# Kernel optimization log

Hardware: AMD Instinct MI355X
Metric: run time of the kernel (lower is better)

## Reference

```python
import jax, jax.numpy as jnp
import numpy as np
from jax import lax

WINDOW_SIZE = 11
SIGMA = 1.5
DATA_RANGE = 2.0


def _gauss_1d(size, sigma):
    coords = np.arange(size, dtype=np.float32) - size // 2
    g = np.exp(-coords ** 2 / (2.0 * sigma ** 2))
    g /= g.sum()
    return jnp.asarray(g)


def _gaussian_filter_2d(x, window):
    # x: (N, C, H, W); separable depthwise Gaussian blur
    C = x.shape[1]
    pad = window.shape[0] // 2
    win_h = jnp.tile(window.reshape(1, 1, 1, -1), (C, 1, 1, 1))  # (C,1,1,K)
    win_v = jnp.tile(window.reshape(1, 1, -1, 1), (C, 1, 1, 1))  # (C,1,K,1)
    dn = ('NCHW', 'OIHW', 'NCHW')
    out = lax.conv_general_dilated(x, win_h, window_strides=(1, 1),
                                   padding=((0, 0), (pad, pad)),
                                   dimension_numbers=dn, feature_group_count=C)
    out = lax.conv_general_dilated(out, win_v, window_strides=(1, 1),
                                   padding=((pad, pad), (0, 0)),
                                   dimension_numbers=dn, feature_group_count=C)
    return out


def _ssim_2d(x, y):
    C1 = (0.01 * DATA_RANGE) ** 2
    C2 = (0.03 * DATA_RANGE) ** 2
    window = _gauss_1d(WINDOW_SIZE, SIGMA).astype(x.dtype)
    mu_x = _gaussian_filter_2d(x, window)
    mu_y = _gaussian_filter_2d(y, window)
    mu_x_sq = mu_x * mu_x
    mu_y_sq = mu_y * mu_y
    mu_xy = mu_x * mu_y
    sigma_x_sq = jnp.maximum(_gaussian_filter_2d(x * x, window) - mu_x_sq, 0.0)
    sigma_y_sq = jnp.maximum(_gaussian_filter_2d(y * y, window) - mu_y_sq, 0.0)
    sigma_xy = _gaussian_filter_2d(x * y, window) - mu_xy
    ssim_map = ((2.0 * mu_xy + C1) * (2.0 * sigma_xy + C2)) / (
        (mu_x_sq + mu_y_sq + C1) * (sigma_x_sq + sigma_y_sq + C2))
    return ssim_map.mean()


def setup_inputs() -> dict:
    key = jax.random.key(0)
    k1, k2 = jax.random.split(key)
    pred = jax.random.normal(k1, (16, 3, 512, 512), dtype=jnp.float32)
    target = jax.random.normal(k2, (16, 3, 512, 512), dtype=jnp.float32)
    return {"pred": pred, "target": target}


def reference(pred, target):
    return 1.0 - _ssim_2d(pred, target)
```

## Files before the change

kernel.cpp:

```cpp
#include <hip/hip_runtime.h>
#include <math.h>


typedef _Float16 f16x8 __attribute__((ext_vector_type(8)));
typedef _Float16 f16x4 __attribute__((ext_vector_type(4)));
typedef float f32x4 __attribute__((ext_vector_type(4)));
typedef _Float16 h2 __attribute__((ext_vector_type(2)));

#define RAWP 88
#define NPIX (16 * 3 * 512 * 512)
#define NBLOCKS (48 * 16 * 8)

union U4 { f16x4 v; h2 p[2]; };
union U8 { f16x8 v; h2 p[4]; };
union UB { unsigned u[4]; f16x8 v; };
union UP { h2 h; unsigned u; };

static __device__ __forceinline__ h2 pkrtz(float a, float b) {
    auto r = __builtin_amdgcn_cvt_pkrtz(a, b);
    union { decltype(r) f; h2 h; } x; x.f = r; return x.h;
}
static __device__ __forceinline__ unsigned pk_u32(float a, float b) {
    UP x; x.h = pkrtz(a, b); return x.u;
}

struct alignas(16) BandTabs { float bh[64][8]; float wv[64][8]; };
static constexpr BandTabs mk_tabs() {
    constexpr float GW[11] = {
        0.00102838f, 0.00759876f, 0.03600026f, 0.10936083f, 0.21300567f,
        0.26601190f, 0.21300567f, 0.10936083f, 0.03600026f, 0.00759876f,
        0.00102838f};
    BandTabs t{};
    for (int lane = 0; lane < 64; ++lane) {
        const int l15 = lane & 15, kg = lane >> 4;
        for (int j = 0; j < 8; ++j) {
            const int kk = kg * 8 + j;
            const int ib = kk - l15 - 3;
            const int iv = kk - l15;
            t.bh[lane][j] = (ib >= 0 && ib < 11) ? GW[ib] : 0.0f;
            t.wv[lane][j] = (iv >= 0 && iv < 11) ? GW[iv] : 0.0f;
        }
    }
    return t;
}
__device__ constexpr BandTabs TAB = mk_tabs();

static __device__ __forceinline__ f16x8 load_band(const float* row) {
    const float4 a = *(const float4*)row;
    const float4 b = *(const float4*)(row + 4);
    U8 r;
    r.p[0] = pkrtz(a.x, a.y); r.p[1] = pkrtz(a.z, a.w);
    r.p[2] = pkrtz(b.x, b.y); r.p[3] = pkrtz(b.z, b.w);
    return r.v;
}

__global__ __launch_bounds__(256, 8) void ssim_main(
    const float* __restrict__ X, const float* __restrict__ Y,
    float* __restrict__ partial)
{
    __shared__ _Float16 rawx[48 * RAWP];
    __shared__ _Float16 rawy[48 * RAWP];
    __shared__ float red[4];

    const int tid = threadIdx.x;
    const int bid = blockIdx.x;

    const int wg    = (bid & 7) * (NBLOCKS / 8) + (bid >> 3);
    const int plane = wg >> 7;
    const int tt    = wg & 127;
    const int tr    = tt >> 3;
    const int tc    = tt & 7;

    const float* xp = X + (size_t)plane * (512 * 512);
    const float* yp = Y + (size_t)plane * (512 * 512);
    const int row0 = tr * 32 - 5;
    const int colT = tc * 64;
    const int colB = colT - 8;

    for (int u = tid; u < 960; u += 256) {
        const int r  = u / 20;
        const int c4 = u - r * 20;
        const int gr = row0 + r;
        const int gc = colB + 4 * c4;
        const bool ok = ((unsigned)gr < 512u) && ((unsigned)gc <= 508u);
        float4 xv = make_float4(0.f, 0.f, 0.f, 0.f), yv = xv;
        if (ok) {
            xv = *(const float4*)(xp + gr * 512 + gc);
            yv = *(const float4*)(yp + gr * 512 + gc);
        }
        U4 tx, ty;
        tx.p[0] = pkrtz(xv.x, xv.y); tx.p[1] = pkrtz(xv.z, xv.w);
        ty.p[0] = pkrtz(yv.x, yv.y); ty.p[1] = pkrtz(yv.z, yv.w);
        *(f16x4*)(rawx + r * RAWP + 4 * c4) = tx.v;
        *(f16x4*)(rawy + r * RAWP + 4 * c4) = ty.v;
    }

    const int w    = tid >> 6;
    const int lane = tid & 63;
    const int l15  = lane & 15;
    const int kg   = lane >> 4;

    const f16x8 BH = load_band(TAB.bh[lane]);
    const f16x8 WV = load_band(TAB.wv[lane]);

    __syncthreads();

    const f32x4 zero4 = {0.f, 0.f, 0.f, 0.f};
    const int rawc = 16 * w + 8 * kg;

    unsigned pq[4][3][2];
#pragma unroll
    for (int mt = 0; mt < 3; ++mt) {
        const int r = mt * 16 + l15;
        const f16x8 fx = *(const f16x8*)(rawx + r * RAWP + rawc);
        const f16x8 fy = *(const f16x8*)(rawy + r * RAWP + rawc);
        const f16x8 fxy = fx * fy;
        const f16x8 fss = fx * fx + fy * fy;

        const f32x4 c0 = __builtin_amdgcn_mfma_f32_16x16x32_f16(fx,  BH, zero4, 0, 0, 0);
        const f32x4 c1 = __builtin_amdgcn_mfma_f32_16x16x32_f16(fy,  BH, zero4, 0, 0, 0);
        const f32x4 c2 = __builtin_amdgcn_mfma_f32_16x16x32_f16(fss, BH, zero4, 0, 0, 0);
        const f32x4 c3 = __builtin_amdgcn_mfma_f32_16x16x32_f16(fxy, BH, zero4, 0, 0, 0);

        pq[0][mt][0] = pk_u32(c0[0], c0[1]); pq[0][mt][1] = pk_u32(c0[2], c0[3]);
        pq[1][mt][0] = pk_u32(c1[0], c1[1]); pq[1][mt][1] = pk_u32(c1[2], c1[3]);
        pq[2][mt][0] = pk_u32(c2[0], c2[1]); pq[2][mt][1] = pk_u32(c2[2], c2[3]);
        pq[3][mt][0] = pk_u32(c3[0], c3[1]); pq[3][mt][1] = pk_u32(c3[2], c3[3]);
    }

    const int addrA = ((2 * (kg & 1)) * 16 + l15) * 4;
    const int addrB = addrA + 64;
    const bool hi = (kg >= 2);

    const float C1 = 0.0004f, C2 = 0.0036f;
    float lsum = 0.f;
#pragma unroll
    for (int mtv = 0; mtv < 2; ++mtv) {
        f32x4 v[4];
#pragma unroll
        for (int q = 0; q < 4; ++q) {
            const unsigned s0 = hi ? pq[q][mtv + 1][0] : pq[q][mtv][0];
            const unsigned s1 = hi ? pq[q][mtv + 1][1] : pq[q][mtv][1];
            UB b;
            b.u[0] = (unsigned)__builtin_amdgcn_ds_bpermute(addrA, (int)s0);
            b.u[1] = (unsigned)__builtin_amdgcn_ds_bpermute(addrA, (int)s1);
            b.u[2] = (unsigned)__builtin_amdgcn_ds_bpermute(addrB, (int)s0);
            b.u[3] = (unsigned)__builtin_amdgcn_ds_bpermute(addrB, (int)s1);
            v[q] = __builtin_amdgcn_mfma_f32_16x16x32_f16(WV, b.v, zero4, 0, 0, 0);
        }
#pragma unroll
        for (int r2 = 0; r2 < 4; ++r2) {
            const float mux = v[0][r2], muy = v[1][r2];
            const float ess = v[2][r2], exy = v[3][r2];
            const float mux2 = mux * mux, muy2 = muy * muy, muxy = mux * muy;
            const float svar = fmaxf(ess - mux2 - muy2, 0.f);
            const float sxy = exy - muxy;
            const float num = (2.f * muxy + C1) * (2.f * sxy + C2);
            const float den = (mux2 + muy2 + C1) * (svar + C2);
            lsum += num * __builtin_amdgcn_rcpf(den);
        }
    }

#pragma unroll
    for (int off = 32; off > 0; off >>= 1)
        lsum += __shfl_down(lsum, off, 64);
    if (lane == 0) red[w] = lsum;
    __syncthreads();
    if (tid == 0)
        partial[bid] = red[0] + red[1] + red[2] + red[3];
}

__global__ void ssim_final(const float* __restrict__ partial,
                           float* __restrict__ out)
{
    const int tid = threadIdx.x;
    double s = 0.0;
    for (int i = tid; i < NBLOCKS; i += 1024) s += (double)partial[i];
#pragma unroll
    for (int off = 32; off > 0; off >>= 1)
        s += __shfl_down(s, off, 64);
    __shared__ double ws[16];
    if ((tid & 63) == 0) ws[tid >> 6] = s;
    __syncthreads();
    if (tid == 0) {
        double tot = 0.0;
#pragma unroll
        for (int i = 0; i < 16; ++i) tot += ws[i];
        out[0] = (float)(1.0 - tot / (double)NPIX);
    }
}

extern "C" void kernel_launch(void* const* d_in, const int* in_sizes, int n_in,
                              void* d_out, int out_size, void* d_ws, size_t ws_size,
                              hipStream_t stream)
{
    const float* x = (const float*)d_in[0];
    const float* y = (const float*)d_in[1];
    float* partial = (float*)d_ws;
    float* out = (float*)d_out;

    ssim_main<<<NBLOCKS, 256, 0, stream>>>(x, y, partial);
    ssim_final<<<1, 1024, 0, stream>>>(partial, out);
}
```

Measured before the change: 32.06 us.

## Give each wave a private LDS panel and drop the block barrier

Each wave now loads its own 48x32 halo panel of x and y straight into registers, all loads issued up front, and writes them to a per-wave LDS region. This replaces the shared block-wide tile that needed a __syncthreads. It removes the block barrier and exposes more memory-level parallelism per wave. In exchange, overlapping halo columns are loaded redundantly across waves (32 columns per 16 output columns), LDS per block grows, and occupancy bounds drop from 8 to 5.

```diff
diff --git a/kernel.cpp b/kernel.cpp
--- a/kernel.cpp
+++ b/kernel.cpp
@@ -7,7 +7,7 @@
 typedef float f32x4 __attribute__((ext_vector_type(4)));
 typedef _Float16 h2 __attribute__((ext_vector_type(2)));
 
-#define RAWP 88
+#define PNP 40
 #define NPIX (16 * 3 * 512 * 512)
 #define NBLOCKS (48 * 16 * 8)
 
@@ -54,12 +54,11 @@
     return r.v;
 }
 
-__global__ __launch_bounds__(256, 8) void ssim_main(
+__global__ __launch_bounds__(256, 5) void ssim_main(
     const float* __restrict__ X, const float* __restrict__ Y,
     float* __restrict__ partial)
 {
-    __shared__ _Float16 rawx[48 * RAWP];
-    __shared__ _Float16 rawy[48 * RAWP];
+    __shared__ _Float16 panel[4][2][48 * PNP];
     __shared__ float red[4];
 
     const int tid = threadIdx.x;
@@ -75,45 +74,50 @@
     const float* yp = Y + (size_t)plane * (512 * 512);
     const int row0 = tr * 32 - 5;
     const int colT = tc * 64;
-    const int colB = colT - 8;
-
-    for (int u = tid; u < 960; u += 256) {
-        const int r  = u / 20;
-        const int c4 = u - r * 20;
-        const int gr = row0 + r;
-        const int gc = colB + 4 * c4;
-        const bool ok = ((unsigned)gr < 512u) && ((unsigned)gc <= 508u);
-        float4 xv = make_float4(0.f, 0.f, 0.f, 0.f), yv = xv;
-        if (ok) {
-            xv = *(const float4*)(xp + gr * 512 + gc);
-            yv = *(const float4*)(yp + gr * 512 + gc);
-        }
-        U4 tx, ty;
-        tx.p[0] = pkrtz(xv.x, xv.y); tx.p[1] = pkrtz(xv.z, xv.w);
-        ty.p[0] = pkrtz(yv.x, yv.y); ty.p[1] = pkrtz(yv.z, yv.w);
-        *(f16x4*)(rawx + r * RAWP + 4 * c4) = tx.v;
-        *(f16x4*)(rawy + r * RAWP + 4 * c4) = ty.v;
-    }
 
     const int w    = tid >> 6;
     const int lane = tid & 63;
     const int l15  = lane & 15;
     const int kg   = lane >> 4;
 
+    const int lr = lane >> 3;
+    const int q8 = lane & 7;
+    const int gcol = colT + 16 * w - 8 + 4 * q8;
+    const bool colOK = (gcol >= 0) && (gcol <= 508);
+
+    const float4 f4z = make_float4(0.f, 0.f, 0.f, 0.f);
+    float4 px[6], py[6];
+#pragma unroll
+    for (int li = 0; li < 6; ++li) {
+        const int gr = row0 + 8 * li + lr;
+        const bool ok = colOK && ((unsigned)gr < 512u);
+        px[li] = ok ? *(const float4*)(xp + gr * 512 + gcol) : f4z;
+        py[li] = ok ? *(const float4*)(yp + gr * 512 + gcol) : f4z;
+    }
+
+    _Float16* pnx = panel[w][0];
+    _Float16* pny = panel[w][1];
+#pragma unroll
+    for (int li = 0; li < 6; ++li) {
+        const int off = (8 * li + lr) * PNP + 4 * q8;
+        U4 tx, ty;
+        tx.p[0] = pkrtz(px[li].x, px[li].y); tx.p[1] = pkrtz(px[li].z, px[li].w);
+        ty.p[0] = pkrtz(py[li].x, py[li].y); ty.p[1] = pkrtz(py[li].z, py[li].w);
+        *(f16x4*)(pnx + off) = tx.v;
+        *(f16x4*)(pny + off) = ty.v;
+    }
+
     const f16x8 BH = load_band(TAB.bh[lane]);
     const f16x8 WV = load_band(TAB.wv[lane]);
 
-    __syncthreads();
-
     const f32x4 zero4 = {0.f, 0.f, 0.f, 0.f};
-    const int rawc = 16 * w + 8 * kg;
 
     unsigned pq[4][3][2];
 #pragma unroll
     for (int mt = 0; mt < 3; ++mt) {
         const int r = mt * 16 + l15;
-        const f16x8 fx = *(const f16x8*)(rawx + r * RAWP + rawc);
-        const f16x8 fy = *(const f16x8*)(rawy + r * RAWP + rawc);
+        const f16x8 fx = *(const f16x8*)(pnx + r * PNP + 8 * kg);
+        const f16x8 fy = *(const f16x8*)(pny + r * PNP + 8 * kg);
         const f16x8 fxy = fx * fy;
         const f16x8 fss = fx * fx + fy * fy;
 
```

After: 75.75 us. +136.3%, slower.
